# Kernel optimization log

Measured on AMD Instinct MI355X. Metric: run time of the kernel, lower is better.

## Reference

```python
import jax, jax.numpy as jnp
from jax import lax
import numpy as np

B, T, H, K = 32, 512, 2048, 128


def setup_inputs() -> dict:
    key = jax.random.key(0)
    k1, k2, k3, k4, k5, k6, k7 = jax.random.split(key, 7)
    hiddens = jax.random.normal(k1, (B, T, H), dtype=jnp.float32)
    mask = jnp.ones((B, T), dtype=jnp.int32)  # mask[:,0] must be on (torchcrf)
    labels = jax.random.randint(k2, (B, T), 0, K)
    W = jax.random.normal(k3, (H, K), dtype=jnp.float32) * 0.02
    b = jnp.zeros((K,), dtype=jnp.float32)
    # torchcrf inits transitions uniform(-0.1, 0.1)
    start_transitions = jax.random.uniform(k4, (K,), minval=-0.1, maxval=0.1)
    end_transitions = jax.random.uniform(k5, (K,), minval=-0.1, maxval=0.1)
    transitions = jax.random.uniform(k6, (K, K), minval=-0.1, maxval=0.1)
    return {"hiddens": hiddens, "mask": mask, "labels": labels, "W": W, "b": b,
            "start_transitions": start_transitions, "end_transitions": end_transitions,
            "transitions": transitions}


def _crf_log_likelihood(emissions, tags, mask, start_t, end_t, trans):
    # emissions: [B,T,K], tags/mask: [B,T]
    Bn, Tn, Kn = emissions.shape
    maskf = mask.astype(emissions.dtype)
    # ---- numerator: score of the gold path ----
    score = start_t[tags[:, 0]] + emissions[jnp.arange(Bn), 0, tags[:, 0]]
    prev, cur = tags[:, :-1], tags[:, 1:]
    emit_cur = jnp.take_along_axis(emissions[:, 1:], cur[..., None], axis=-1)[..., 0]
    score = score + jnp.sum((trans[prev, cur] + emit_cur) * maskf[:, 1:], axis=1)
    last_idx = mask.sum(axis=1).astype(jnp.int32) - 1
    last_tags = jnp.take_along_axis(tags, last_idx[:, None], axis=1)[:, 0]
    score = score + end_t[last_tags]
    # ---- denominator: log partition via stable logsumexp scan ----
    def step(alpha, inp):
        emit_t, m_t = inp  # [B,K], [B]
        nxt = jax.nn.logsumexp(alpha[:, :, None] + trans[None] + emit_t[:, None, :], axis=1)
        alpha = jnp.where(m_t[:, None] > 0, nxt, alpha)
        return alpha, None
    alpha0 = start_t[None, :] + emissions[:, 0]
    emits = jnp.swapaxes(emissions[:, 1:], 0, 1)  # [T-1,B,K]
    ms = jnp.swapaxes(mask[:, 1:], 0, 1)          # [T-1,B]
    alpha, _ = lax.scan(step, alpha0, (emits, ms))
    logZ = jax.nn.logsumexp(alpha + end_t[None, :], axis=1)
    return score - logZ


def _viterbi_decode(emissions, mask, start_t, end_t, trans):
    Bn, Tn, Kn = emissions.shape
    tag_ids = jnp.arange(Kn, dtype=jnp.int32)
    def step(score, inp):
        emit_t, m_t = inp
        cand = score[:, :, None] + trans[None]          # [B,K,K] prev->cur
        bp = jnp.argmax(cand, axis=1).astype(jnp.int32)  # [B,K]
        best = jnp.max(cand, axis=1) + emit_t
        on = m_t[:, None] > 0
        new_score = jnp.where(on, best, score)
        bp = jnp.where(on, bp, tag_ids[None, :])  # identity for padded steps
        return new_score, bp
    score0 = start_t[None, :] + emissions[:, 0]
    emits = jnp.swapaxes(emissions[:, 1:], 0, 1)
    ms = jnp.swapaxes(mask[:, 1:], 0, 1)
    score, history = lax.scan(step, score0, (emits, ms))  # history: [T-1,B,K]
    last_tag = jnp.argmax(score + end_t[None, :], axis=1).astype(jnp.int32)  # [B]
    def back(tag, bp_t):
        tag = jnp.take_along_axis(bp_t, tag[:, None], axis=1)[:, 0]
        return tag, tag
    _, tags_prev = lax.scan(back, last_tag, history, reverse=True)  # [T-1,B]
    tags = jnp.concatenate([tags_prev, last_tag[None, :]], axis=0)  # [T,B]
    return jnp.swapaxes(tags, 0, 1)  # [B,T]


def reference(hiddens, mask, labels, W, b, start_transitions, end_transitions, transitions):
    logits = jnp.einsum('bth,hk->btk', hiddens, W) + b  # emission projection
    decode = _viterbi_decode(logits, mask, start_transitions, end_transitions, transitions)
    llh = _crf_log_likelihood(logits, labels, mask, start_transitions, end_transitions, transitions)
    loss = -jnp.mean(llh)  # -1 * crf(..., reduction='mean')
    return (decode, loss)
```

## Files before the change

kernel.cpp:

```cpp
#include <hip/hip_runtime.h>
#include <hip/hip_bf16.h>
#include <math.h>

#define BB 32
#define TT 512
#define HH 2048
#define KK 128
#define CH 8

__global__ __launch_bounds__(512) void gemm_k(const float* __restrict__ hid,
                                              const float* __restrict__ Wm,
                                              const float* __restrict__ bias,
                                              float* __restrict__ logits,
                                              float* __restrict__ loss_slot) {
    __shared__ union {
        struct { float As[4][16][72]; float Bs[4][16][132]; } s;
        float4 red[16][128];
    } sm;
    const int tid = threadIdx.x, bid = blockIdx.x;
    if (bid == 0 && tid == 0) loss_slot[0] = 0.0f;
    const int g = tid >> 7, lt = tid & 127;
    const int rowBase = bid * 64;
    const int rowg = lt >> 4, colg = lt & 15;
    const int arow = lt >> 1, ahq = lt & 1;

    float acc[8][8];
#pragma unroll
    for (int i = 0; i < 8; i++)
#pragma unroll
        for (int j = 0; j < 8; j++) acc[i][j] = 0.0f;

    const float* hA = hid + (size_t)(rowBase + arow) * HH + g * 512 + ahq * 8;

    float4 a0, a1, bv[4];
    {
        const int h0 = g * 512;
        a0 = *(const float4*)(hA);
        a1 = *(const float4*)(hA + 4);
#pragma unroll
        for (int r = 0; r < 4; ++r) {
            int idx = r * 128 + lt;
            bv[r] = *(const float4*)(Wm + (size_t)(h0 + (idx >> 5)) * KK + (idx & 31) * 4);
        }
    }

    for (int it = 0; it < 32; ++it) {
        __syncthreads();
        const int hb = ahq * 8;
        sm.s.As[g][hb + 0][arow] = a0.x;
        sm.s.As[g][hb + 1][arow] = a0.y;
        sm.s.As[g][hb + 2][arow] = a0.z;
        sm.s.As[g][hb + 3][arow] = a0.w;
        sm.s.As[g][hb + 4][arow] = a1.x;
        sm.s.As[g][hb + 5][arow] = a1.y;
        sm.s.As[g][hb + 6][arow] = a1.z;
        sm.s.As[g][hb + 7][arow] = a1.w;
#pragma unroll
        for (int r = 0; r < 4; ++r) {
            int idx = r * 128 + lt;
            *(float4*)&sm.s.Bs[g][idx >> 5][(idx & 31) * 4] = bv[r];
        }
        __syncthreads();
        if (it + 1 < 32) {
            const int h0 = g * 512 + (it + 1) * 16;
            a0 = *(const float4*)(hA + (it + 1) * 16);
            a1 = *(const float4*)(hA + (it + 1) * 16 + 4);
#pragma unroll
            for (int r = 0; r < 4; ++r) {
                int idx = r * 128 + lt;
                bv[r] = *(const float4*)(Wm + (size_t)(h0 + (idx >> 5)) * KK + (idx & 31) * 4);
            }
        }
#pragma unroll
        for (int h = 0; h < 16; ++h) {
            float4 aL = *(const float4*)&sm.s.As[g][h][rowg * 8];
            float4 aH = *(const float4*)&sm.s.As[g][h][rowg * 8 + 4];
            float4 b0 = *(const float4*)&sm.s.Bs[g][h][colg * 4];
            float4 b1 = *(const float4*)&sm.s.Bs[g][h][64 + colg * 4];
            float ar[8] = {aL.x, aL.y, aL.z, aL.w, aH.x, aH.y, aH.z, aH.w};
            float br[8] = {b0.x, b0.y, b0.z, b0.w, b1.x, b1.y, b1.z, b1.w};
#pragma unroll
            for (int i = 0; i < 8; i++)
#pragma unroll
                for (int j = 0; j < 8; j++) acc[i][j] = fmaf(ar[i], br[j], acc[i][j]);
        }
    }
    __syncthreads();
    for (int gp = 1; gp <= 3; ++gp) {
        if (g == gp) {
#pragma unroll
            for (int i = 0; i < 8; ++i) {
                sm.red[i * 2][lt] = make_float4(acc[i][0], acc[i][1], acc[i][2], acc[i][3]);
                sm.red[i * 2 + 1][lt] = make_float4(acc[i][4], acc[i][5], acc[i][6], acc[i][7]);
            }
        }
        __syncthreads();
        if (g == 0) {
#pragma unroll
            for (int i = 0; i < 8; ++i) {
                float4 r0 = sm.red[i * 2][lt];
                float4 r1 = sm.red[i * 2 + 1][lt];
                acc[i][0] += r0.x; acc[i][1] += r0.y; acc[i][2] += r0.z; acc[i][3] += r0.w;
                acc[i][4] += r1.x; acc[i][5] += r1.y; acc[i][6] += r1.z; acc[i][7] += r1.w;
            }
        }
        __syncthreads();
    }
    if (g == 0) {
        float4 bb0 = *(const float4*)(bias + colg * 4);
        float4 bb1 = *(const float4*)(bias + 64 + colg * 4);
#pragma unroll
        for (int i = 0; i < 8; ++i) {
            int row = rowBase + rowg * 8 + i;
            *(float4*)(logits + (size_t)row * KK + colg * 4) =
                make_float4(acc[i][0] + bb0.x, acc[i][1] + bb0.y, acc[i][2] + bb0.z, acc[i][3] + bb0.w);
            *(float4*)(logits + (size_t)row * KK + 64 + colg * 4) =
                make_float4(acc[i][4] + bb1.x, acc[i][5] + bb1.y, acc[i][6] + bb1.z, acc[i][7] + bb1.w);
        }
    }
}

struct SMemB {
    float ubuf[2][144];
    float em[2][CH * KK];
    float red[4];
    float vbuf[128];
};

__global__ __launch_bounds__(256) void scan_k(const float* __restrict__ logits,
                                              const int* __restrict__ mask,
                                              const int* __restrict__ labels,
                                              const float* __restrict__ startT,
                                              const float* __restrict__ endT,
                                              const float* __restrict__ trans,
                                              float* __restrict__ shist,
                                              float* __restrict__ out) {
    __shared__ SMemB sm;
    const int tid = threadIdx.x;
    const int bid = blockIdx.x;
    const float L2E = 1.4426950408889634f;
    const int s = tid & 3;
    const int jb = tid >> 2;
    const int j0 = jb * 2;
    const int padw = j0 + 4 * (j0 >> 5);
    const int lane = tid & 63;
    const int NCHUNK = TT / CH;

    if (bid < BB) {
        const int b = bid;
        const float* lrow = logits + (size_t)b * TT * KK;
        unsigned long long mb[8];
#pragma unroll
        for (int c = 0; c < 8; ++c) mb[c] = __ballot(mask[b * TT + c * 64 + lane]);
        float V0[32], V1[32];
#pragma unroll
        for (int k = 0; k < 32; k++) {
            V0[k] = exp2f(trans[(s * 32 + k) * KK + j0] * L2E);
            V1[k] = exp2f(trans[(s * 32 + k) * KK + j0 + 1] * L2E);
        }
        float a0_ = (startT[j0] + lrow[j0]) * L2E;
        float a1_ = (startT[j0 + 1] + lrow[j0 + 1]) * L2E;
        float OFF = (startT[0] + lrow[0]) * L2E;
        float S0_ = exp2f(a0_ - OFF);
        float S1_ = exp2f(a1_ - OFF);
        if (s == 0) {
            sm.ubuf[0][padw] = S0_;
            sm.ubuf[0][padw + 1] = S1_;
        }
        float4 st = *(const float4*)(lrow + tid * 4);
        *(float4*)&sm.em[0][tid * 4] = st;
        __syncthreads();
        int cur = 0;
        for (int c = 0; c < NCHUNK; ++c) {
            const int buf = c & 1;
#pragma unroll
            for (int r = 0; r < CH; ++r) {
                const int t = c * CH + r;
                if (r == 0 && c + 1 < NCHUNK)
                    st = *(const float4*)(lrow + (size_t)(c + 1) * CH * KK + tid * 4);
                if (t > 0) {
                    int mt = (int)((mb[t >> 6] >> (t & 63)) & 1ull);
                    if (mt) {
                        float2 em = *(const float2*)&sm.em[buf][r * KK + j0];
                        const float* ub = &sm.ubuf[cur][s * 36];
                        float u00 = sm.ubuf[cur][0];
                        float uu[32];
#pragma unroll
                        for (int cc = 0; cc < 8; ++cc) {
                            float4 v = *(const float4*)(ub + cc * 4);
                            uu[cc * 4] = v.x; uu[cc * 4 + 1] = v.y; uu[cc * 4 + 2] = v.z; uu[cc * 4 + 3] = v.w;
                        }
                        float r00 = __builtin_amdgcn_rcpf(u00);
                        OFF += log2f(u00);
                        float sc0 = exp2f(em.x * L2E) * r00;
                        float sc1 = exp2f(em.y * L2E) * r00;
                        float p0[4] = {0.f, 0.f, 0.f, 0.f}, p1[4] = {0.f, 0.f, 0.f, 0.f};
#pragma unroll
                        for (int k = 0; k < 32; k += 4) {
#pragma unroll
                            for (int q = 0; q < 4; ++q) {
                                p0[q] = fmaf(uu[k + q], V0[k + q], p0[q]);
                                p1[q] = fmaf(uu[k + q], V1[k + q], p1[q]);
                            }
                        }
                        float w0 = (p0[0] + p0[1]) + (p0[2] + p0[3]);
                        float w1 = (p1[0] + p1[1]) + (p1[2] + p1[3]);
                        w0 += __shfl_xor(w0, 1, 64);
                        w0 += __shfl_xor(w0, 2, 64);
                        w1 += __shfl_xor(w1, 1, 64);
                        w1 += __shfl_xor(w1, 2, 64);
                        S0_ = w0 * sc0;
                        S1_ = w1 * sc1;
                        if (s == 0) {
                            sm.ubuf[cur ^ 1][padw] = S0_;
                            sm.ubuf[cur ^ 1][padw + 1] = S1_;
                        }
                        cur ^= 1;
                    }
                }
                if (r == CH - 1 && c + 1 < NCHUNK)
                    *(float4*)&sm.em[buf ^ 1][tid * 4] = st;
                __syncthreads();
            }
        }
        if (s == 0) {
            sm.vbuf[j0] = log2f(S0_) + endT[j0] * L2E;
            sm.vbuf[j0 + 1] = log2f(S1_) + endT[j0 + 1] * L2E;
        }
        __syncthreads();

        float part = 0.0f;
        for (int tt = tid; tt < TT; tt += 256) {
            if (tt == 0) {
                int l0 = labels[b * TT];
                part += startT[l0] + lrow[l0];
            } else if (mask[b * TT + tt]) {
                int lc = labels[b * TT + tt];
                int lp = labels[b * TT + tt - 1];
                part += trans[lp * KK + lc] + lrow[(size_t)tt * KK + lc];
            }
        }
#pragma unroll
        for (int d = 1; d < 64; d <<= 1) part += __shfl_xor(part, d, 64);
        int wid = tid >> 6;
        if (lane == 0) sm.red[wid] = part;
        __syncthreads();
        if (tid < 64) {
            float v0 = sm.vbuf[tid], v1 = sm.vbuf[tid + 64];
            float mx = fmaxf(v0, v1);
#pragma unroll
            for (int d = 1; d < 64; d <<= 1) mx = fmaxf(mx, __shfl_xor(mx, d, 64));
            float p = exp2f(v0 - mx) + exp2f(v1 - mx);
#pragma unroll
            for (int d = 1; d < 64; d <<= 1) p += __shfl_xor(p, d, 64);
            if (tid == 0) {
                int total = 0;
#pragma unroll
                for (int c = 0; c < 8; ++c) total += __popcll(mb[c]);
                float score = sm.red[0] + sm.red[1] + sm.red[2] + sm.red[3];
                score += endT[labels[b * TT + total - 1]];
                float logZ = (OFF + mx + log2f(p)) * 0.6931471805599453f;
                float llh = score - logZ;
                atomicAdd(out + BB * TT, -llh * (1.0f / 32.0f));
            }
        }
    } else {
        const int b = bid - BB;
        const float* lrow = logits + (size_t)b * TT * KK;
        float* hist = shist + (size_t)b * TT * KK;
        unsigned long long mb[8];
#pragma unroll
        for (int c = 0; c < 8; ++c) mb[c] = __ballot(mask[b * TT + c * 64 + lane]);
        float T0[32], T1[32];
#pragma unroll
        for (int k = 0; k < 32; k++) {
            T0[k] = trans[(s * 32 + k) * KK + j0];
            T1[k] = trans[(s * 32 + k) * KK + j0 + 1];
        }
        float s0_ = startT[j0] + lrow[j0];
        float s1_ = startT[j0 + 1] + lrow[j0 + 1];
        if (s == 0) {
            sm.ubuf[0][padw] = s0_;
            sm.ubuf[0][padw + 1] = s1_;
        }
        float4 st = *(const float4*)(lrow + tid * 4);
        *(float4*)&sm.em[0][tid * 4] = st;
        __syncthreads();
        int cur = 0;
        float2 hb[CH];
        for (int c = 0; c < NCHUNK; ++c) {
            const int buf = c & 1;
#pragma unroll
            for (int r = 0; r < CH; ++r) {
                const int t = c * CH + r;
                if (r == 0 && c + 1 < NCHUNK)
                    st = *(const float4*)(lrow + (size_t)(c + 1) * CH * KK + tid * 4);
                if (t > 0) {
                    int mt = (int)((mb[t >> 6] >> (t & 63)) & 1ull);
                    if (mt) {
                        float2 em = *(const float2*)&sm.em[buf][r * KK + j0];
                        const float* ub = &sm.ubuf[cur][s * 36];
                        float uu[32];
#pragma unroll
                        for (int cc = 0; cc < 8; ++cc) {
                            float4 v = *(const float4*)(ub + cc * 4);
                            uu[cc * 4] = v.x; uu[cc * 4 + 1] = v.y; uu[cc * 4 + 2] = v.z; uu[cc * 4 + 3] = v.w;
                        }
                        float m0a = -3.0e38f, m0b = -3.0e38f, m1a = -3.0e38f, m1b = -3.0e38f;
#pragma unroll
                        for (int k = 0; k < 32; k += 4) {
                            m0a = fmaxf(m0a, fmaxf(uu[k] + T0[k], uu[k + 1] + T0[k + 1]));
                            m0b = fmaxf(m0b, fmaxf(uu[k + 2] + T0[k + 2], uu[k + 3] + T0[k + 3]));
                            m1a = fmaxf(m1a, fmaxf(uu[k] + T1[k], uu[k + 1] + T1[k + 1]));
                            m1b = fmaxf(m1b, fmaxf(uu[k + 2] + T1[k + 2], uu[k + 3] + T1[k + 3]));
                        }
                        float m0 = fmaxf(m0a, m0b), m1 = fmaxf(m1a, m1b);
                        m0 = fmaxf(m0, __shfl_xor(m0, 1, 64));
                        m0 = fmaxf(m0, __shfl_xor(m0, 2, 64));
                        m1 = fmaxf(m1, __shfl_xor(m1, 1, 64));
                        m1 = fmaxf(m1, __shfl_xor(m1, 2, 64));
                        s0_ = m0 + em.x;
                        s1_ = m1 + em.y;
                        if (s == 0) {
                            sm.ubuf[cur ^ 1][padw] = s0_;
                            sm.ubuf[cur ^ 1][padw + 1] = s1_;
                        }
                        cur ^= 1;
                    }
                }
                hb[r] = make_float2(s0_, s1_);
                if (r == CH - 1 && c + 1 < NCHUNK)
                    *(float4*)&sm.em[buf ^ 1][tid * 4] = st;
                __syncthreads();
            }
            if (s == 1) {
#pragma unroll
                for (int r = 0; r < CH; ++r)
                    *(float2*)(hist + (size_t)(c * CH + r) * KK + j0) = hb[r];
            }
        }
    }
}

__global__ __launch_bounds__(256) void bp_k(const float* __restrict__ shist,
                                            const float* __restrict__ trans,
                                            const int* __restrict__ mask,
                                            unsigned char* __restrict__ bp) {
    const int t = blockIdx.x + 1;
    const int tid = threadIdx.x;
    const int j = tid & 127, bg = tid >> 7;
    __shared__ float sc[BB][KK];
#pragma unroll
    for (int r = 0; r < 4; ++r) {
        int f = tid + r * 256;
        int bb2 = f >> 5, c4 = (f & 31) * 4;
        *(float4*)&sc[bb2][c4] = *(const float4*)&shist[(size_t)bb2 * TT * KK + (size_t)(t - 1) * KK + c4];
    }
    __syncthreads();
    float m[16];
    int idx[16];
#pragma unroll
    for (int c = 0; c < 16; c++) { m[c] = -3.0e38f; idx[c] = 0; }
    for (int i4 = 0; i4 < 32; ++i4) {
        const int ib = i4 * 4;
        float tr0 = trans[(ib + 0) * KK + j];
        float tr1 = trans[(ib + 1) * KK + j];
        float tr2 = trans[(ib + 2) * KK + j];
        float tr3 = trans[(ib + 3) * KK + j];
#pragma unroll
        for (int c = 0; c < 16; c++) {
            float4 s4 = *(const float4*)&sc[bg + 2 * c][ib];
            float c0 = s4.x + tr0, c1 = s4.y + tr1, c2 = s4.z + tr2, c3 = s4.w + tr3;
            if (c0 > m[c]) { m[c] = c0; idx[c] = ib; }
            if (c1 > m[c]) { m[c] = c1; idx[c] = ib + 1; }
            if (c2 > m[c]) { m[c] = c2; idx[c] = ib + 2; }
            if (c3 > m[c]) { m[c] = c3; idx[c] = ib + 3; }
        }
    }
#pragma unroll
    for (int c = 0; c < 16; c++) {
        int bb2 = bg + 2 * c;
        int v = idx[c];
        if (mask[bb2 * TT + t] == 0) v = j;
        bp[(size_t)bb2 * TT * KK + (size_t)t * KK + j] = (unsigned char)v;
    }
}

__global__ __launch_bounds__(512) void bt_k(const float* __restrict__ shist,
                                            const float* __restrict__ endT,
                                            const unsigned char* __restrict__ bp,
                                            float* __restrict__ out) {
    const int b = blockIdx.x;
    const int tid = threadIdx.x;
    const int lane = tid & 63, w = tid >> 6;
    __shared__ float cb[128];
    __shared__ int tagbuf[512];
    __shared__ int handoff;
    if (tid < 128) cb[tid] = shist[(size_t)b * TT * KK + (size_t)(TT - 1) * KK + tid] + endT[tid];
    __syncthreads();
    if (tid == 0) {
        float mm = cb[0];
        int bi = 0;
        for (int i = 1; i < 128; i++)
            if (cb[i] > mm) { mm = cb[i]; bi = i; }
        tagbuf[TT - 1] = bi;
        handoff = bi;
    }
    unsigned int reg[64];
    const unsigned char* bpb = bp + (size_t)b * TT * KK;
#pragma unroll
    for (int r = 0; r < 64; r++) {
        int t_row = w * 64 + 1 + r;
        unsigned int v = 0;
        if (t_row < TT) v = *(const unsigned short*)(bpb + (size_t)t_row * KK + lane * 2);
        reg[r] = v;
    }
    __syncthreads();
    for (int ph = 7; ph >= 0; --ph) {
        if (w == ph) {
            int tag = handoff;
#pragma unroll
            for (int r = 63; r >= 0; --r) {
                int t_row = ph * 64 + 1 + r;
                if (t_row < TT) {
                    unsigned int vv = (unsigned int)__shfl((int)reg[r], tag >> 1, 64);
                    tag = (int)((vv >> ((tag & 1) * 8)) & 0xffu);
                    if (lane == 0) tagbuf[t_row - 1] = tag;
                }
            }
            if (lane == 0) handoff = tag;
        }
        __syncthreads();
    }
    out[b * TT + tid] = (float)tagbuf[tid];
}

extern "C" void kernel_launch(void* const* d_in, const int* in_sizes, int n_in,
                              void* d_out, int out_size, void* d_ws, size_t ws_size,
                              hipStream_t stream) {
    const float* hid = (const float*)d_in[0];
    const int* mask = (const int*)d_in[1];
    const int* labels = (const int*)d_in[2];
    const float* Wm = (const float*)d_in[3];
    const float* bias = (const float*)d_in[4];
    const float* startT = (const float*)d_in[5];
    const float* endT = (const float*)d_in[6];
    const float* trans = (const float*)d_in[7];
    float* out = (float*)d_out;
    char* ws = (char*)d_ws;

    float* logits = (float*)ws;
    float* shist = (float*)(ws + 8388608);
    unsigned char* bp = (unsigned char*)(ws + 16777216);

    gemm_k<<<256, 512, 0, stream>>>(hid, Wm, bias, logits, out + BB * TT);
    scan_k<<<64, 256, 0, stream>>>(logits, mask, labels, startT, endT, trans, shist, out);
    bp_k<<<TT - 1, 256, 0, stream>>>(shist, trans, mask, bp);
    bt_k<<<BB, 512, 0, stream>>>(shist, endT, bp, out);
}
```

Before: 657.2 us.

## Prefetch emissions into registers and use DPP quad reductions in CRF scans

The forward-algorithm and Viterbi scan loops no longer stage emission chunks through shared memory. Each thread prefetches its own float2 emissions for the next chunk into registers, which removes the shared-memory em buffer and its store. Cross-lane shuffles for the 4-lane reductions are replaced with DPP quad_perm adds and maxes, and the forward dot product uses two accumulators instead of four. It also writes the t=0 Viterbi history row explicitly and sets launch bounds to one block. The cost is more registers for the prefetch buffers, and the per-step latency on the serial scan is expected to drop.

```diff
diff --git a/kernel.cpp b/kernel.cpp
--- a/kernel.cpp
+++ b/kernel.cpp
@@ -7,6 +7,21 @@
 #define HH 2048
 #define KK 128
 #define CH 8
+
+__device__ __forceinline__ float quad_add(float x) {
+    int a = __builtin_amdgcn_update_dpp(0, __float_as_int(x), 0xB1, 0xF, 0xF, true);
+    x += __int_as_float(a);
+    int b = __builtin_amdgcn_update_dpp(0, __float_as_int(x), 0x4E, 0xF, 0xF, true);
+    x += __int_as_float(b);
+    return x;
+}
+__device__ __forceinline__ float quad_max(float x) {
+    int a = __builtin_amdgcn_update_dpp(0, __float_as_int(x), 0xB1, 0xF, 0xF, true);
+    x = fmaxf(x, __int_as_float(a));
+    int b = __builtin_amdgcn_update_dpp(0, __float_as_int(x), 0x4E, 0xF, 0xF, true);
+    x = fmaxf(x, __int_as_float(b));
+    return x;
+}
 
 __global__ __launch_bounds__(512) void gemm_k(const float* __restrict__ hid,
                                               const float* __restrict__ Wm,
@@ -122,19 +137,18 @@
 
 struct SMemB {
     float ubuf[2][144];
-    float em[2][CH * KK];
     float red[4];
     float vbuf[128];
 };
 
-__global__ __launch_bounds__(256) void scan_k(const float* __restrict__ logits,
-                                              const int* __restrict__ mask,
-                                              const int* __restrict__ labels,
-                                              const float* __restrict__ startT,
-                                              const float* __restrict__ endT,
-                                              const float* __restrict__ trans,
-                                              float* __restrict__ shist,
-                                              float* __restrict__ out) {
+__global__ __launch_bounds__(256, 1) void scan_k(const float* __restrict__ logits,
+                                                 const int* __restrict__ mask,
+                                                 const int* __restrict__ labels,
+                                                 const float* __restrict__ startT,
+                                                 const float* __restrict__ endT,
+                                                 const float* __restrict__ trans,
+                                                 float* __restrict__ shist,
+                                                 float* __restrict__ out) {
     __shared__ SMemB sm;
     const int tid = threadIdx.x;
     const int bid = blockIdx.x;
@@ -151,7 +165,7 @@
         const float* lrow = logits + (size_t)b * TT * KK;
         unsigned long long mb[8];
 #pragma unroll
-        for (int c = 0; c < 8; ++c) mb[c] = __ballot(mask[b * TT + c * 64 + lane]);
+        for (int c = 0; c < 8; ++c) mb[c] = __ballot(mask[b * TT + c * 64 + lane] != 0);
         float V0[32], V1[32];
 #pragma unroll
         for (int k = 0; k < 32; k++) {
@@ -167,61 +181,54 @@
             sm.ubuf[0][padw] = S0_;
             sm.ubuf[0][padw + 1] = S1_;
         }
-        float4 st = *(const float4*)(lrow + tid * 4);
-        *(float4*)&sm.em[0][tid * 4] = st;
+        float2 emc[CH], emn[CH];
+#pragma unroll
+        for (int d = 0; d < CH; ++d) emc[d] = *(const float2*)(lrow + (size_t)d * KK + j0);
         __syncthreads();
         int cur = 0;
         for (int c = 0; c < NCHUNK; ++c) {
-            const int buf = c & 1;
 #pragma unroll
             for (int r = 0; r < CH; ++r) {
                 const int t = c * CH + r;
-                if (r == 0 && c + 1 < NCHUNK)
-                    st = *(const float4*)(lrow + (size_t)(c + 1) * CH * KK + tid * 4);
-                if (t > 0) {
-                    int mt = (int)((mb[t >> 6] >> (t & 63)) & 1ull);
-                    if (mt) {
-                        float2 em = *(const float2*)&sm.em[buf][r * KK + j0];
-                        const float* ub = &sm.ubuf[cur][s * 36];
-                        float u00 = sm.ubuf[cur][0];
-                        float uu[32];
-#pragma unroll
-                        for (int cc = 0; cc < 8; ++cc) {
-                            float4 v = *(const float4*)(ub + cc * 4);
-                            uu[cc * 4] = v.x; uu[cc * 4 + 1] = v.y; uu[cc * 4 + 2] = v.z; uu[cc * 4 + 3] = v.w;
-                        }
-                        float r00 = __builtin_amdgcn_rcpf(u00);
-                        OFF += log2f(u00);
-                        float sc0 = exp2f(em.x * L2E) * r00;
-                        float sc1 = exp2f(em.y * L2E) * r00;
-                        float p0[4] = {0.f, 0.f, 0.f, 0.f}, p1[4] = {0.f, 0.f, 0.f, 0.f};
-#pragma unroll
-                        for (int k = 0; k < 32; k += 4) {
-#pragma unroll
-                            for (int q = 0; q < 4; ++q) {
-                                p0[q] = fmaf(uu[k + q], V0[k + q], p0[q]);
-                                p1[q] = fmaf(uu[k + q], V1[k + q], p1[q]);
-                            }
-                        }
-                        float w0 = (p0[0] + p0[1]) + (p0[2] + p0[3]);
-                        float w1 = (p1[0] + p1[1]) + (p1[2] + p1[3]);
-                        w0 += __shfl_xor(w0, 1, 64);
-                        w0 += __shfl_xor(w0, 2, 64);
-                        w1 += __shfl_xor(w1, 1, 64);
-                        w1 += __shfl_xor(w1, 2, 64);
-                        S0_ = w0 * sc0;
-                        S1_ = w1 * sc1;
-                        if (s == 0) {
-                            sm.ubuf[cur ^ 1][padw] = S0_;
-                            sm.ubuf[cur ^ 1][padw + 1] = S1_;
-                        }
-                        cur ^= 1;
-                    }
+                if (r == 0 && c + 1 < NCHUNK) {
+#pragma unroll
+                    for (int d = 0; d < CH; ++d)
+                        emn[d] = *(const float2*)(lrow + (size_t)((c + 1) * CH + d) * KK + j0);
                 }
-                if (r == CH - 1 && c + 1 < NCHUNK)
-                    *(float4*)&sm.em[buf ^ 1][tid * 4] = st;
+                if (t > 0 && ((mb[t >> 6] >> (t & 63)) & 1ull)) {
+                    const float* ub = &sm.ubuf[cur][s * 36];
+                    float u00 = sm.ubuf[cur][0];
+                    float uu[32];
+#pragma unroll
+                    for (int cc = 0; cc < 8; ++cc) {
+                        float4 v = *(const float4*)(ub + cc * 4);
+                        uu[cc * 4] = v.x; uu[cc * 4 + 1] = v.y; uu[cc * 4 + 2] = v.z; uu[cc * 4 + 3] = v.w;
+                    }
+                    float2 em = emc[r];
+                    float p0e = 0.f, p0o = 0.f, p1e = 0.f, p1o = 0.f;
+#pragma unroll
+                    for (int k = 0; k < 32; k += 2) {
+                        p0e = fmaf(uu[k], V0[k], p0e);
+                        p1e = fmaf(uu[k], V1[k], p1e);
+                        p0o = fmaf(uu[k + 1], V0[k + 1], p0o);
+                        p1o = fmaf(uu[k + 1], V1[k + 1], p1o);
+                    }
+                    float w0 = quad_add(p0e + p0o);
+                    float w1 = quad_add(p1e + p1o);
+                    float rinv = __builtin_amdgcn_rcpf(u00);
+                    OFF += log2f(u00);
+                    S0_ = w0 * (exp2f(em.x * L2E) * rinv);
+                    S1_ = w1 * (exp2f(em.y * L2E) * rinv);
+                    if (s == 0) {
+                        sm.ubuf[cur ^ 1][padw] = S0_;
+                        sm.ubuf[cur ^ 1][padw + 1] = S1_;
+                    }
+                    cur ^= 1;
+                }
                 __syncthreads();
             }
+#pragma unroll
+            for (int d = 0; d < CH; ++d) emc[d] = emn[d];
         }
         if (s == 0) {
             sm.vbuf[j0] = log2f(S0_) + endT[j0] * L2E;
@@ -270,7 +277,7 @@
         float* hist = shist + (size_t)b * TT * KK;
         unsigned long long mb[8];
 #pragma unroll
-        for (int c = 0; c < 8; ++c) mb[c] = __ballot(mask[b * TT + c * 64 + lane]);
+        for (int c = 0; c < 8; ++c) mb[c] = __ballot(mask[b * TT + c * 64 + lane] != 0);
         float T0[32], T1[32];
 #pragma unroll
         for (int k = 0; k < 32; k++) {
@@ -282,55 +289,51 @@
         if (s == 0) {
             sm.ubuf[0][padw] = s0_;
             sm.ubuf[0][padw + 1] = s1_;
-        }
-        float4 st = *(const float4*)(lrow + tid * 4);
-        *(float4*)&sm.em[0][tid * 4] = st;
+        } else if (s == 1) {
+            *(float2*)(hist + j0) = make_float2(s0_, s1_);
+        }
+        float2 emc[CH], emn[CH], hb[CH];
+#pragma unroll
+        for (int d = 0; d < CH; ++d) emc[d] = *(const float2*)(lrow + (size_t)d * KK + j0);
         __syncthreads();
         int cur = 0;
-        float2 hb[CH];
         for (int c = 0; c < NCHUNK; ++c) {
-            const int buf = c & 1;
 #pragma unroll
             for (int r = 0; r < CH; ++r) {
                 const int t = c * CH + r;
-                if (r == 0 && c + 1 < NCHUNK)
-                    st = *(const float4*)(lrow + (size_t)(c + 1) * CH * KK + tid * 4);
-                if (t > 0) {
-                    int mt = (int)((mb[t >> 6] >> (t & 63)) & 1ull);
-                    if (mt) {
-                        float2 em = *(const float2*)&sm.em[buf][r * KK + j0];
-                        const float* ub = &sm.ubuf[cur][s * 36];
-                        float uu[32];
-#pragma unroll
-                        for (int cc = 0; cc < 8; ++cc) {
-                            float4 v = *(const float4*)(ub + cc * 4);
-                            uu[cc * 4] = v.x; uu[cc * 4 + 1] = v.y; uu[cc * 4 + 2] = v.z; uu[cc * 4 + 3] = v.w;
-                        }
-                        float m0a = -3.0e38f, m0b = -3.0e38f, m1a = -3.0e38f, m1b = -3.0e38f;
-#pragma unroll
-                        for (int k = 0; k < 32; k += 4) {
-                            m0a = fmaxf(m0a, fmaxf(uu[k] + T0[k], uu[k + 1] + T0[k + 1]));
-                            m0b = fmaxf(m0b, fmaxf(uu[k + 2] + T0[k + 2], uu[k + 3] + T0[k + 3]));
-                            m1a = fmaxf(m1a, fmaxf(uu[k] + T1[k], uu[k + 1] + T1[k + 1]));
-                            m1b = fmaxf(m1b, fmaxf(uu[k + 2] + T1[k + 2], uu[k + 3] + T1[k + 3]));
-                        }
-                        float m0 = fmaxf(m0a, m0b), m1 = fmaxf(m1a, m1b);
-                        m0 = fmaxf(m0, __shfl_xor(m0, 1, 64));
-                        m0 = fmaxf(m0, __shfl_xor(m0, 2, 64));
-                        m1 = fmaxf(m1, __shfl_xor(m1, 1, 64));
-                        m1 = fmaxf(m1, __shfl_xor(m1, 2, 64));
-                        s0_ = m0 + em.x;
-                        s1_ = m1 + em.y;
-                        if (s == 0) {
-                            sm.ubuf[cur ^ 1][padw] = s0_;
-                            sm.ubuf[cur ^ 1][padw + 1] = s1_;
-                        }
-                        cur ^= 1;
-                    }
+                if (r == 0 && c + 1 < NCHUNK) {
+#pragma unroll
+                    for (int d = 0; d < CH; ++d)
+                        emn[d] = *(const float2*)(lrow + (size_t)((c + 1) * CH + d) * KK + j0);
+                }
+                if (t > 0 && ((mb[t >> 6] >> (t & 63)) & 1ull)) {
+                    const float* ub = &sm.ubuf[cur][s * 36];
+                    float uu[32];
+#pragma unroll
+                    for (int cc = 0; cc < 8; ++cc) {
+                        float4 v = *(const float4*)(ub + cc * 4);
+                        uu[cc * 4] = v.x; uu[cc * 4 + 1] = v.y; uu[cc * 4 + 2] = v.z; uu[cc * 4 + 3] = v.w;
+                    }
+                    float2 em = emc[r];
+                    float m0a = -3.0e38f, m0b = -3.0e38f, m1a = -3.0e38f, m1b = -3.0e38f;
+#pragma unroll
+                    for (int k = 0; k < 32; k += 4) {
+                        m0a = fmaxf(m0a, fmaxf(uu[k] + T0[k], uu[k + 1] + T0[k + 1]));
+                        m0b = fmaxf(m0b, fmaxf(uu[k + 2] + T0[k + 2], uu[k + 3] + T0[k + 3]));
+                        m1a = fmaxf(m1a, fmaxf(uu[k] + T1[k], uu[k + 1] + T1[k + 1]));
+                        m1b = fmaxf(m1b, fmaxf(uu[k + 2] + T1[k + 2], uu[k + 3] + T1[k + 3]));
+                    }
+                    float m0 = quad_max(fmaxf(m0a, m0b));
+                    float m1 = quad_max(fmaxf(m1a, m1b));
+                    s0_ = m0 + em.x;
+                    s1_ = m1 + em.y;
+                    if (s == 0) {
+                        sm.ubuf[cur ^ 1][padw] = s0_;
+                        sm.ubuf[cur ^ 1][padw + 1] = s1_;
+                    }
+                    cur ^= 1;
                 }
                 hb[r] = make_float2(s0_, s1_);
-                if (r == CH - 1 && c + 1 < NCHUNK)
-                    *(float4*)&sm.em[buf ^ 1][tid * 4] = st;
                 __syncthreads();
             }
             if (s == 1) {
@@ -338,6 +341,8 @@
                 for (int r = 0; r < CH; ++r)
                     *(float2*)(hist + (size_t)(c * CH + r) * KK + j0) = hb[r];
             }
+#pragma unroll
+            for (int d = 0; d < CH; ++d) emc[d] = emn[d];
         }
     }
 }
```

Result: faster. 620.1 us (-5.6%).
